# Performance work log

Measured on AMD Instinct MI355X. Metric: run time of the kernel, lower is better.

## Reference

```python
import jax, jax.numpy as jnp
import numpy as np


def setup_inputs() -> dict:
    key = jax.random.key(0)
    ks = jax.random.split(key, 5)
    B, C, H, W = 16, 512, 32, 32
    n_heads, d_k = 4, 128
    return {
        "x": jax.random.normal(ks[0], (B, C, H, W), dtype=jnp.float32),
        "w_proj": jax.random.normal(ks[1], (3 * n_heads * d_k, C), dtype=jnp.float32) * (1.0 / np.sqrt(C)),
        "b_proj": jax.random.normal(ks[2], (3 * n_heads * d_k,), dtype=jnp.float32) * 0.01,
        "w_out": jax.random.normal(ks[3], (C, n_heads * d_k), dtype=jnp.float32) * (1.0 / np.sqrt(n_heads * d_k)),
        "b_out": jax.random.normal(ks[4], (C,), dtype=jnp.float32) * 0.01,
        "n_heads": n_heads,
    }


def reference(x, w_proj, b_proj, w_out, b_out, n_heads):
    B, C, H, W = x.shape
    seq = H * W
    d_k = (w_proj.shape[0] // 3) // n_heads
    scale = d_k ** -0.5

    xs = x.reshape(B, C, seq).transpose(0, 2, 1)          # [B, seq, C]
    qkv = xs @ w_proj.T + b_proj                           # [B, seq, 3*H*d_k]
    qkv = qkv.reshape(B, seq, n_heads, 3 * d_k)
    q, k, v = jnp.split(qkv, 3, axis=-1)                   # each [B, seq, H, d_k]

    attn = jnp.einsum('bihd,bjhd->bijh', q, k) * scale     # [B, seq, seq, H]
    # NOTE: softmax over the QUERY axis (dim=1), faithful to the source quirk.
    attn = jax.nn.softmax(attn, axis=1)

    res = jnp.einsum('bijh,bjhd->bihd', attn, v)           # [B, seq, H, d_k]
    res = res.reshape(B, seq, n_heads * d_k)
    res = res @ w_out.T + b_out + xs                       # residual add
    return res.transpose(0, 2, 1).reshape(B, C, H, W)
```

## Files before the change

### kernel.cpp

```cpp
#include <hip/hip_runtime.h>
#include <hip/hip_bf16.h>
#include <math.h>

#define B_    16
#define CIN   512
#define SEQ   1024
#define NH    4
#define DK    128
#define OUT3  1536
#define SCALE 0.08838834764831845f

typedef __attribute__((ext_vector_type(8))) __bf16 bf16x8;
typedef __attribute__((ext_vector_type(4))) float f32x4;

#define MFMA(a, b, c) __builtin_amdgcn_mfma_f32_16x16x32_bf16((a), (b), (c), 0, 0, 0)

__device__ __forceinline__ ushort f2bf(float f) {
    __hip_bfloat16 h = __float2bfloat16(f);
    return *(ushort*)&h;
}
__device__ __forceinline__ uint pk2(float a, float b) {
    return (uint)f2bf(a) | ((uint)f2bf(b) << 16);
}
__device__ __forceinline__ void g2l16(const ushort* g, ushort* l) {
    __builtin_amdgcn_global_load_lds(
        (const __attribute__((address_space(1))) unsigned int*)g,
        (__attribute__((address_space(3))) unsigned int*)l, 16, 0, 0);
}
__device__ __forceinline__ int xcdswz(int bid, int nwg) {
    return (bid & 7) * (nwg >> 3) + (bid >> 3);
}

__global__ __launch_bounds__(256) void transpose_cast_kernel(
    const float* __restrict__ x, ushort* __restrict__ xt)
{
    __shared__ ushort t[64 * 66];
    const int tid = threadIdx.x;
    const int i0 = blockIdx.x * 64, c0 = blockIdx.y * 64, b = blockIdx.z;

    #pragma unroll
    for (int l = 0; l < 4; ++l) {
        int idx = tid + l * 256;
        int c = idx >> 4, i4 = (idx & 15) << 2;
        float4 v = *(const float4*)&x[((size_t)b * CIN + c0 + c) * SEQ + i0 + i4];
        t[(i4 + 0) * 66 + c] = f2bf(v.x);
        t[(i4 + 1) * 66 + c] = f2bf(v.y);
        t[(i4 + 2) * 66 + c] = f2bf(v.z);
        t[(i4 + 3) * 66 + c] = f2bf(v.w);
    }
    __syncthreads();
    #pragma unroll
    for (int l = 0; l < 4; ++l) {
        int idx = tid + l * 256;
        int i = idx >> 4, c4 = (idx & 15) << 2;
        uint2 p;
        p.x = *(const uint*)&t[i * 66 + c4];
        p.y = *(const uint*)&t[i * 66 + c4 + 2];
        *(uint2*)&xt[((size_t)b * SEQ + i0 + i) * CIN + c0 + c4] = p;
    }
}

__global__ __launch_bounds__(256) void cast_kernel(
    const float* __restrict__ src, ushort* __restrict__ dst, int n4)
{
    int idx = blockIdx.x * 256 + threadIdx.x;
    if (idx < n4) {
        float4 v = *(const float4*)&src[(size_t)idx * 4];
        uint2 p; p.x = pk2(v.x, v.y); p.y = pk2(v.z, v.w);
        *(uint2*)&dst[(size_t)idx * 4] = p;
    }
}

__global__ __launch_bounds__(256) void qkv_kernel(
    const ushort* __restrict__ wbf, const float* __restrict__ bias,
    const ushort* __restrict__ xt,
    ushort* __restrict__ qb, ushort* __restrict__ kb, ushort* __restrict__ vtb)
{
    __shared__ __attribute__((aligned(16))) ushort lds_a[128 * 32];
    __shared__ __attribute__((aligned(16))) ushort lds_b[128 * 32];
    const int tid = threadIdx.x;
    const int lane = tid & 63, wv = tid >> 6;
    const int l15 = lane & 15, l4 = lane >> 4;
    const int wm = wv >> 1, wn = wv & 1;
    const int swz = xcdswz(blockIdx.x, 1536);
    const int o0 = (swz % 12) * 128;
    const int i0 = ((swz / 12) & 7) * 128;
    const int b  = swz / 96;

    f32x4 acc[4][4] = {};
    for (int c0 = 0; c0 < CIN; c0 += 32) {
        __syncthreads();
        #pragma unroll
        for (int l = 0; l < 2; ++l) {
            int chunk = l * 256 + tid;
            int row = chunk >> 2, c = chunk & 3;
            g2l16(&wbf[(size_t)(o0 + row) * CIN + c0 + (c << 3)],
                  &lds_a[(size_t)(l * 256 + wv * 64) * 8]);
        }
        #pragma unroll
        for (int l = 0; l < 2; ++l) {
            int chunk = l * 256 + tid;
            int row = chunk >> 2, c = chunk & 3;
            g2l16(&xt[((size_t)b * SEQ + i0 + row) * CIN + c0 + (c << 3)],
                  &lds_b[(size_t)(l * 256 + wv * 64) * 8]);
        }
        __syncthreads();
        bf16x8 af[4], bfv[4];
        #pragma unroll
        for (int m = 0; m < 4; ++m)
            af[m] = *(const bf16x8*)&lds_a[(wm * 64 + m * 16 + l15) * 32 + (l4 << 3)];
        #pragma unroll
        for (int n = 0; n < 4; ++n)
            bfv[n] = *(const bf16x8*)&lds_b[(wn * 64 + n * 16 + l15) * 32 + (l4 << 3)];
        #pragma unroll
        for (int m = 0; m < 4; ++m)
            #pragma unroll
            for (int n = 0; n < 4; ++n)
                acc[m][n] = MFMA(af[m], bfv[n], acc[m][n]);
    }
    const int h = o0 / 384, which = (o0 % 384) / 128;
    const int bh = b * NH + h;
    #pragma unroll
    for (int m = 0; m < 4; ++m) {
        const int d0 = wm * 64 + m * 16 + (l4 << 2);
        float bia[4];
        #pragma unroll
        for (int r = 0; r < 4; ++r) bia[r] = bias[o0 + d0 + r];
        #pragma unroll
        for (int n = 0; n < 4; ++n) {
            const int i = i0 + wn * 64 + n * 16 + l15;
            float v0 = acc[m][n][0] + bia[0], v1 = acc[m][n][1] + bia[1];
            float v2 = acc[m][n][2] + bia[2], v3 = acc[m][n][3] + bia[3];
            if (which == 2) {
                vtb[((size_t)bh * DK + d0 + 0) * SEQ + i] = f2bf(v0);
                vtb[((size_t)bh * DK + d0 + 1) * SEQ + i] = f2bf(v1);
                vtb[((size_t)bh * DK + d0 + 2) * SEQ + i] = f2bf(v2);
                vtb[((size_t)bh * DK + d0 + 3) * SEQ + i] = f2bf(v3);
            } else {
                ushort* dst = (which == 0) ? qb : kb;
                uint2 p; p.x = pk2(v0, v1); p.y = pk2(v2, v3);
                *(uint2*)&dst[((size_t)bh * SEQ + i) * DK + d0] = p;
            }
        }
    }
}

__global__ __launch_bounds__(256) void stats_kernel(
    const ushort* __restrict__ qb, const ushort* __restrict__ kb,
    float* __restrict__ mstat, float* __restrict__ rstat)
{
    __shared__ __attribute__((aligned(16))) ushort lds_q[64 * 128];
    const int tid = threadIdx.x;
    const int lane = tid & 63, wv = tid >> 6;
    const int l15 = lane & 15, l4 = lane >> 4;
    const int swz = xcdswz(blockIdx.x, 512);
    const int bh = swz >> 3;
    const int j0 = (swz & 7) * 128 + wv * 32;
    const ushort* kbase = kb + (size_t)bh * SEQ * DK;
    const ushort* qbase = qb + (size_t)bh * SEQ * DK;

    bf16x8 kf[2][4];
    #pragma unroll
    for (int m = 0; m < 2; ++m)
        #pragma unroll
        for (int ks = 0; ks < 4; ++ks)
            kf[m][ks] = *(const bf16x8*)&kbase[(size_t)(j0 + m * 16 + l15) * DK
                                               + ks * 32 + (l4 << 3)];
    float mm[2][4], ss[2][4];
    #pragma unroll
    for (int m = 0; m < 2; ++m)
        #pragma unroll
        for (int r = 0; r < 4; ++r) { mm[m][r] = -1e30f; ss[m][r] = 0.0f; }

    for (int it = 0; it < SEQ / 64; ++it) {
        __syncthreads();
        #pragma unroll
        for (int l = 0; l < 4; ++l) {
            int chunk = l * 256 + tid;
            int row = chunk >> 4, c = chunk & 15;
            g2l16(&qbase[(size_t)(it * 64 + row) * DK + ((c ^ (row & 7)) << 3)],
                  &lds_q[(size_t)(l * 256 + wv * 64) * 8]);
        }
        __syncthreads();
        f32x4 sa0[4], sa1[4];
        #pragma unroll
        for (int n = 0; n < 4; ++n) {
            f32x4 a0 = {}, a1 = {};
            #pragma unroll
            for (int ks = 0; ks < 4; ++ks) {
                bf16x8 bq = *(const bf16x8*)&lds_q[(n * 16 + l15) * 128
                                + ((((ks << 2) | l4) ^ (l15 & 7)) << 3)];
                a0 = MFMA(kf[0][ks], bq, a0);
                a1 = MFMA(kf[1][ks], bq, a1);
            }
            sa0[n] = a0; sa1[n] = a1;
        }
        #pragma unroll
        for (int r = 0; r < 4; ++r) {
            {
                float v0 = sa0[0][r] * SCALE, v1 = sa0[1][r] * SCALE;
                float v2 = sa0[2][r] * SCALE, v3 = sa0[3][r] * SCALE;
                float tm = fmaxf(fmaxf(v0, v1), fmaxf(v2, v3));
                float nm = fmaxf(mm[0][r], tm);
                float s4 = __expf(v0 - nm) + __expf(v1 - nm)
                         + __expf(v2 - nm) + __expf(v3 - nm);
                ss[0][r] = ss[0][r] * __expf(mm[0][r] - nm) + s4;
                mm[0][r] = nm;
            }
            {
                float v0 = sa1[0][r] * SCALE, v1 = sa1[1][r] * SCALE;
                float v2 = sa1[2][r] * SCALE, v3 = sa1[3][r] * SCALE;
                float tm = fmaxf(fmaxf(v0, v1), fmaxf(v2, v3));
                float nm = fmaxf(mm[1][r], tm);
                float s4 = __expf(v0 - nm) + __expf(v1 - nm)
                         + __expf(v2 - nm) + __expf(v3 - nm);
                ss[1][r] = ss[1][r] * __expf(mm[1][r] - nm) + s4;
                mm[1][r] = nm;
            }
        }
    }
    #pragma unroll
    for (int m = 0; m < 2; ++m)
        #pragma unroll
        for (int r = 0; r < 4; ++r) {
            float mv = mm[m][r], sv = ss[m][r];
            #pragma unroll
            for (int wmask = 1; wmask < 16; wmask <<= 1) {
                float mo = __shfl_xor(mv, wmask, 64);
                float so = __shfl_xor(sv, wmask, 64);
                float mn = fmaxf(mv, mo);
                sv = sv * __expf(mv - mn) + so * __expf(mo - mn);
                mv = mn;
            }
            if (l15 == 0) {
                int j = j0 + m * 16 + (l4 << 2) + r;
                mstat[(size_t)bh * SEQ + j] = mv;
                rstat[(size_t)bh * SEQ + j] = 1.0f / sv;
            }
        }
}

__global__ __launch_bounds__(256) void attn_kernel(
    const ushort* __restrict__ qb, const ushort* __restrict__ kb,
    const ushort* __restrict__ vtb,
    const float* __restrict__ mstat, const float* __restrict__ rstat,
    ushort* __restrict__ resb)
{
    __shared__ __attribute__((aligned(16))) ushort lds_k[64 * 128];
    __shared__ __attribute__((aligned(16))) ushort lds_vt[128 * 64];
    __shared__ __attribute__((aligned(16))) ushort lds_p[64 * 72];
    const int tid = threadIdx.x;
    const int lane = tid & 63, wv = tid >> 6;
    const int l15 = lane & 15, l4 = lane >> 4;
    const int wj = wv & 1, wi = wv >> 1;
    const int swz = xcdswz(blockIdx.x, 1024);
    const int bh = swz >> 4, b = bh >> 2, h = bh & 3;
    const int i0 = (swz & 15) * 64;
    const ushort* qbase = qb + (size_t)bh * SEQ * DK;
    const ushort* kbase = kb + (size_t)bh * SEQ * DK;
    const ushort* vtbase = vtb + (size_t)bh * DK * SEQ;

    bf16x8 qf[2][4];
    #pragma unroll
    for (int n = 0; n < 2; ++n)
        #pragma unroll
        for (int ks = 0; ks < 4; ++ks)
            qf[n][ks] = *(const bf16x8*)&qbase[(size_t)(i0 + wi * 32 + n * 16 + l15) * DK
                                               + ks * 32 + (l4 << 3)];
    f32x4 oacc[2][4] = {};

    for (int jt = 0; jt < SEQ / 64; ++jt) {
        const int j0 = jt * 64;
        __syncthreads();
        #pragma unroll
        for (int l = 0; l < 4; ++l) {
            int chunk = l * 256 + tid;
            int row = chunk >> 4, c = chunk & 15;
            g2l16(&kbase[(size_t)(j0 + row) * DK + ((c ^ (row & 7)) << 3)],
                  &lds_k[(size_t)(l * 256 + wv * 64) * 8]);
        }
        #pragma unroll
        for (int l = 0; l < 4; ++l) {
            int chunk = l * 256 + tid;
            int row = chunk >> 3, c = chunk & 7;
            g2l16(&vtbase[(size_t)row * SEQ + j0 + ((c ^ (row & 7)) << 3)],
                  &lds_vt[(size_t)(l * 256 + wv * 64) * 8]);
        }
        __syncthreads();
        float mj[2][4], rj[2][4];
        #pragma unroll
        for (int m = 0; m < 2; ++m)
            #pragma unroll
            for (int r = 0; r < 4; ++r) {
                int j = j0 + wj * 32 + m * 16 + (l4 << 2) + r;
                mj[m][r] = mstat[(size_t)bh * SEQ + j];
                rj[m][r] = rstat[(size_t)bh * SEQ + j];
            }
        bf16x8 af[2][4];
        #pragma unroll
        for (int m = 0; m < 2; ++m)
            #pragma unroll
            for (int ks = 0; ks < 4; ++ks)
                af[m][ks] = *(const bf16x8*)&lds_k[(wj * 32 + m * 16 + l15) * 128
                                + ((((ks << 2) | l4) ^ (l15 & 7)) << 3)];
        #pragma unroll
        for (int m = 0; m < 2; ++m)
            #pragma unroll
            for (int n = 0; n < 2; ++n) {
                f32x4 s = {};
                #pragma unroll
                for (int ks = 0; ks < 4; ++ks)
                    s = MFMA(af[m][ks], qf[n][ks], s);
                const int i = wi * 32 + n * 16 + l15;
                float p0 = __expf(s[0] * SCALE - mj[m][0]) * rj[m][0];
                float p1 = __expf(s[1] * SCALE - mj[m][1]) * rj[m][1];
                float p2 = __expf(s[2] * SCALE - mj[m][2]) * rj[m][2];
                float p3 = __expf(s[3] * SCALE - mj[m][3]) * rj[m][3];
                uint2 pp; pp.x = pk2(p0, p1); pp.y = pk2(p2, p3);
                *(uint2*)&lds_p[i * 72 + wj * 32 + m * 16 + (l4 << 2)] = pp;
            }
        __syncthreads();
        #pragma unroll
        for (int ks = 0; ks < 2; ++ks) {
            bf16x8 va0 = *(const bf16x8*)&lds_vt[(wv * 32 + l15) * 64
                            + ((((ks << 2) | l4) ^ (l15 & 7)) << 3)];
            bf16x8 va1 = *(const bf16x8*)&lds_vt[(wv * 32 + 16 + l15) * 64
                            + ((((ks << 2) | l4) ^ (l15 & 7)) << 3)];
            #pragma unroll
            for (int n = 0; n < 4; ++n) {
                bf16x8 pb = *(const bf16x8*)&lds_p[(n * 16 + l15) * 72
                                + ks * 32 + (l4 << 3)];
                oacc[0][n] = MFMA(va0, pb, oacc[0][n]);
                oacc[1][n] = MFMA(va1, pb, oacc[1][n]);
            }
        }
    }
    #pragma unroll
    for (int m = 0; m < 2; ++m)
        #pragma unroll
        for (int n = 0; n < 4; ++n) {
            const int i = i0 + n * 16 + l15;
            const int d = wv * 32 + m * 16 + (l4 << 2);
            uint2 p;
            p.x = pk2(oacc[m][n][0], oacc[m][n][1]);
            p.y = pk2(oacc[m][n][2], oacc[m][n][3]);
            *(uint2*)&resb[((size_t)b * SEQ + i) * (NH * DK) + h * DK + d] = p;
        }
}

__global__ __launch_bounds__(256) void outproj_kernel(
    const ushort* __restrict__ resb, const ushort* __restrict__ woutbf,
    const float* __restrict__ bout, const float* __restrict__ x,
    float* __restrict__ out)
{
    __shared__ __attribute__((aligned(16))) ushort lds_a[128 * 32];
    __shared__ __attribute__((aligned(16))) ushort lds_b[128 * 32];
    const int tid = threadIdx.x;
    const int lane = tid & 63, wv = tid >> 6;
    const int l15 = lane & 15, l4 = lane >> 4;
    const int wm = wv >> 1, wn = wv & 1;
    const int swz = xcdswz(blockIdx.x, 512);
    const int i0 = (swz & 7) * 128;
    const int c0 = ((swz >> 3) & 3) * 128;
    const int b  = swz >> 5;

    f32x4 acc[4][4] = {};
    for (int k0 = 0; k0 < NH * DK; k0 += 32) {
        __syncthreads();
        #pragma unroll
        for (int l = 0; l < 2; ++l) {
            int chunk = l * 256 + tid;
            int row = chunk >> 2, c = chunk & 3;
            g2l16(&woutbf[(size_t)(c0 + row) * (NH * DK) + k0 + (c << 3)],
                  &lds_a[(size_t)(l * 256 + wv * 64) * 8]);
        }
        #pragma unroll
        for (int l = 0; l < 2; ++l) {
            int chunk = l * 256 + tid;
            int row = chunk >> 2, c = chunk & 3;
            g2l16(&resb[((size_t)b * SEQ + i0 + row) * (NH * DK) + k0 + (c << 3)],
                  &lds_b[(size_t)(l * 256 + wv * 64) * 8]);
        }
        __syncthreads();
        bf16x8 af[4], bfv[4];
        #pragma unroll
        for (int m = 0; m < 4; ++m)
            af[m] = *(const bf16x8*)&lds_a[(wm * 64 + m * 16 + l15) * 32 + (l4 << 3)];
        #pragma unroll
        for (int n = 0; n < 4; ++n)
            bfv[n] = *(const bf16x8*)&lds_b[(wn * 64 + n * 16 + l15) * 32 + (l4 << 3)];
        #pragma unroll
        for (int m = 0; m < 4; ++m)
            #pragma unroll
            for (int n = 0; n < 4; ++n)
                acc[m][n] = MFMA(af[m], bfv[n], acc[m][n]);
    }
    #pragma unroll
    for (int m = 0; m < 4; ++m) {
        const int cb = c0 + wm * 64 + m * 16 + (l4 << 2);
        float bia[4];
        #pragma unroll
        for (int r = 0; r < 4; ++r) bia[r] = bout[cb + r];
        #pragma unroll
        for (int n = 0; n < 4; ++n) {
            const int i = i0 + wn * 64 + n * 16 + l15;
            #pragma unroll
            for (int r = 0; r < 4; ++r) {
                size_t off = ((size_t)b * CIN + cb + r) * SEQ + i;
                out[off] = acc[m][n][r] + bia[r] + x[off];
            }
        }
    }
}

extern "C" void kernel_launch(void* const* d_in, const int* in_sizes, int n_in,
                              void* d_out, int out_size, void* d_ws, size_t ws_size,
                              hipStream_t stream) {
    const float* x      = (const float*)d_in[0];
    const float* w_proj = (const float*)d_in[1];
    const float* b_proj = (const float*)d_in[2];
    const float* w_out  = (const float*)d_in[3];
    const float* b_out  = (const float*)d_in[4];

    const size_t xtE = (size_t)B_ * SEQ * CIN;
    const size_t qkE = (size_t)B_ * NH * SEQ * DK;
    ushort* xt    = (ushort*)d_ws;
    ushort* qb    = xt + xtE;
    ushort* kb    = qb + qkE;
    ushort* vtb   = kb + qkE;
    float*  mstat = (float*)(vtb + qkE);
    float*  rstat = mstat + (size_t)B_ * NH * SEQ;
    ushort* resb  = (ushort*)(rstat + (size_t)B_ * NH * SEQ);
    ushort* wobf  = resb + (size_t)B_ * SEQ * (NH * DK);
    ushort* wpbf  = resb;
    float*  out   = (float*)d_out;

    transpose_cast_kernel<<<dim3(SEQ / 64, CIN / 64, B_), 256, 0, stream>>>(x, xt);
    cast_kernel<<<dim3(768), 256, 0, stream>>>(w_proj, wpbf, 196608);
    cast_kernel<<<dim3(256), 256, 0, stream>>>(w_out, wobf, 65536);
    qkv_kernel<<<dim3(1536), 256, 0, stream>>>(wpbf, b_proj, xt, qb, kb, vtb);
    stats_kernel<<<dim3(512), 256, 0, stream>>>(qb, kb, mstat, rstat);
    attn_kernel<<<dim3(1024), 256, 0, stream>>>(qb, kb, vtb, mstat, rstat, resb);
    outproj_kernel<<<dim3(512), 256, 0, stream>>>(resb, wobf, b_out, x, out);
}
```

Before: 259.7 us.

## Double-buffer LDS staging in GEMM and stats kernels, fold softmax stats into logsumexp

The QKV and output projection GEMMs and the stats kernel now double-buffer their LDS tiles, issuing the next tile's global-to-LDS copy before computing on the current one, which removes one barrier per iteration. The attention kernel splits K and V staging so the next K tile loads during the PV MFMA phase, and it wraps the MFMA sections in s_setprio hints. The per-column max and reciprocal sum are merged into one logsumexp value, which removes a load and a multiply per element. The extra LDS buffers double shared memory use in the GEMMs and may lower occupancy.

Result: faster. 250.2 us (-3.7%).

```diff
diff --git a/kernel.cpp b/kernel.cpp
--- a/kernel.cpp
+++ b/kernel.cpp
@@ -76,8 +76,10 @@
     const ushort* __restrict__ xt,
     ushort* __restrict__ qb, ushort* __restrict__ kb, ushort* __restrict__ vtb)
 {
-    __shared__ __attribute__((aligned(16))) ushort lds_a[128 * 32];
-    __shared__ __attribute__((aligned(16))) ushort lds_b[128 * 32];
+    __shared__ __attribute__((aligned(16))) ushort lds_a0[128 * 32];
+    __shared__ __attribute__((aligned(16))) ushort lds_a1[128 * 32];
+    __shared__ __attribute__((aligned(16))) ushort lds_b0[128 * 32];
+    __shared__ __attribute__((aligned(16))) ushort lds_b1[128 * 32];
     const int tid = threadIdx.x;
     const int lane = tid & 63, wv = tid >> 6;
     const int l15 = lane & 15, l4 = lane >> 4;
@@ -87,36 +89,45 @@
     const int i0 = ((swz / 12) & 7) * 128;
     const int b  = swz / 96;
 
-    f32x4 acc[4][4] = {};
-    for (int c0 = 0; c0 < CIN; c0 += 32) {
-        __syncthreads();
+    auto stage = [&](int c0, ushort* la, ushort* lb) {
         #pragma unroll
         for (int l = 0; l < 2; ++l) {
             int chunk = l * 256 + tid;
             int row = chunk >> 2, c = chunk & 3;
             g2l16(&wbf[(size_t)(o0 + row) * CIN + c0 + (c << 3)],
-                  &lds_a[(size_t)(l * 256 + wv * 64) * 8]);
+                  &la[(size_t)(l * 256 + wv * 64) * 8]);
         }
         #pragma unroll
         for (int l = 0; l < 2; ++l) {
             int chunk = l * 256 + tid;
             int row = chunk >> 2, c = chunk & 3;
             g2l16(&xt[((size_t)b * SEQ + i0 + row) * CIN + c0 + (c << 3)],
-                  &lds_b[(size_t)(l * 256 + wv * 64) * 8]);
-        }
-        __syncthreads();
+                  &lb[(size_t)(l * 256 + wv * 64) * 8]);
+        }
+    };
+
+    f32x4 acc[4][4] = {};
+    stage(0, lds_a0, lds_b0);
+    __syncthreads();
+    for (int it = 0; it < CIN / 32; ++it) {
+        const ushort* la = (it & 1) ? lds_a1 : lds_a0;
+        const ushort* lb = (it & 1) ? lds_b1 : lds_b0;
+        if (it + 1 < CIN / 32)
+            stage((it + 1) * 32, (it & 1) ? lds_a0 : lds_a1,
+                                 (it & 1) ? lds_b0 : lds_b1);
         bf16x8 af[4], bfv[4];
         #pragma unroll
         for (int m = 0; m < 4; ++m)
-            af[m] = *(const bf16x8*)&lds_a[(wm * 64 + m * 16 + l15) * 32 + (l4 << 3)];
+            af[m] = *(const bf16x8*)&la[(wm * 64 + m * 16 + l15) * 32 + (l4 << 3)];
         #pragma unroll
         for (int n = 0; n < 4; ++n)
-            bfv[n] = *(const bf16x8*)&lds_b[(wn * 64 + n * 16 + l15) * 32 + (l4 << 3)];
+            bfv[n] = *(const bf16x8*)&lb[(wn * 64 + n * 16 + l15) * 32 + (l4 << 3)];
         #pragma unroll
         for (int m = 0; m < 4; ++m)
             #pragma unroll
             for (int n = 0; n < 4; ++n)
                 acc[m][n] = MFMA(af[m], bfv[n], acc[m][n]);
+        __syncthreads();
     }
     const int h = o0 / 384, which = (o0 % 384) / 128;
     const int bh = b * NH + h;
@@ -147,9 +158,10 @@
 
 __global__ __launch_bounds__(256) void stats_kernel(
     const ushort* __restrict__ qb, const ushort* __restrict__ kb,
-    float* __restrict__ mstat, float* __restrict__ rstat)
-{
-    __shared__ __attribute__((aligned(16))) ushort lds_q[64 * 128];
+    float* __restrict__ cstat)
+{
+    __shared__ __attribute__((aligned(16))) ushort lds_q0[64 * 128];
+    __shared__ __attribute__((aligned(16))) ushort lds_q1[64 * 128];
     const int tid = threadIdx.x;
     const int lane = tid & 63, wv = tid >> 6;
     const int l15 = lane & 15, l4 = lane >> 4;
@@ -159,6 +171,16 @@
     const ushort* kbase = kb + (size_t)bh * SEQ * DK;
     const ushort* qbase = qb + (size_t)bh * SEQ * DK;
 
+    auto stageQ = [&](int it, ushort* dst) {
+        #pragma unroll
+        for (int l = 0; l < 4; ++l) {
+            int chunk = l * 256 + tid;
+            int row = chunk >> 4, c = chunk & 15;
+            g2l16(&qbase[(size_t)(it * 64 + row) * DK + ((c ^ (row & 7)) << 3)],
+                  &dst[(size_t)(l * 256 + wv * 64) * 8]);
+        }
+    };
+
     bf16x8 kf[2][4];
     #pragma unroll
     for (int m = 0; m < 2; ++m)
@@ -172,29 +194,27 @@
         #pragma unroll
         for (int r = 0; r < 4; ++r) { mm[m][r] = -1e30f; ss[m][r] = 0.0f; }
 
+    stageQ(0, lds_q0);
+    __syncthreads();
     for (int it = 0; it < SEQ / 64; ++it) {
-        __syncthreads();
-        #pragma unroll
-        for (int l = 0; l < 4; ++l) {
-            int chunk = l * 256 + tid;
-            int row = chunk >> 4, c = chunk & 15;
-            g2l16(&qbase[(size_t)(it * 64 + row) * DK + ((c ^ (row & 7)) << 3)],
-                  &lds_q[(size_t)(l * 256 + wv * 64) * 8]);
-        }
-        __syncthreads();
+        const ushort* lq = (it & 1) ? lds_q1 : lds_q0;
+        if (it + 1 < SEQ / 64)
+            stageQ(it + 1, (it & 1) ? lds_q0 : lds_q1);
         f32x4 sa0[4], sa1[4];
+        __builtin_amdgcn_s_setprio(1);
         #pragma unroll
         for (int n = 0; n < 4; ++n) {
             f32x4 a0 = {}, a1 = {};
             #pragma unroll
             for (int ks = 0; ks < 4; ++ks) {
-                bf16x8 bq = *(const bf16x8*)&lds_q[(n * 16 + l15) * 128
+                bf16x8 bq = *(const bf16x8*)&lq[(n * 16 + l15) * 128
                                 + ((((ks << 2) | l4) ^ (l15 & 7)) << 3)];
                 a0 = MFMA(kf[0][ks], bq, a0);
                 a1 = MFMA(kf[1][ks], bq, a1);
             }
             sa0[n] = a0; sa1[n] = a1;
         }
+        __builtin_amdgcn_s_setprio(0);
         #pragma unroll
         for (int r = 0; r < 4; ++r) {
             {
@@ -218,6 +238,7 @@
                 mm[1][r] = nm;
             }
         }
+        __syncthreads();
     }
     #pragma unroll
     for (int m = 0; m < 2; ++m)
@@ -234,16 +255,14 @@
             }
             if (l15 == 0) {
                 int j = j0 + m * 16 + (l4 << 2) + r;
-                mstat[(size_t)bh * SEQ + j] = mv;
-                rstat[(size_t)bh * SEQ + j] = 1.0f / sv;
+                cstat[(size_t)bh * SEQ + j] = mv + __logf(sv);
             }
         }
 }
 
 __global__ __launch_bounds__(256) void attn_kernel(
     const ushort* __restrict__ qb, const ushort* __restrict__ kb,
-    const ushort* __restrict__ vtb,
-    const float* __restrict__ mstat, const float* __restrict__ rstat,
+    const ushort* __restrict__ vtb, const float* __restrict__ cstat,
     ushort* __restrict__ resb)
 {
     __shared__ __attribute__((aligned(16))) ushort lds_k[64 * 128];
@@ -259,6 +278,26 @@
     const ushort* qbase = qb + (size_t)bh * SEQ * DK;
     const ushort* kbase = kb + (size_t)bh * SEQ * DK;
     const ushort* vtbase = vtb + (size_t)bh * DK * SEQ;
+    const float* cbase = cstat + (size_t)bh * SEQ;
+
+    auto stageK = [&](int j0t) {
+        #pragma unroll
+        for (int l = 0; l < 4; ++l) {
+            int chunk = l * 256 + tid;
+            int row = chunk >> 4, c = chunk & 15;
+            g2l16(&kbase[(size_t)(j0t + row) * DK + ((c ^ (row & 7)) << 3)],
+                  &lds_k[(size_t)(l * 256 + wv * 64) * 8]);
+        }
+    };
+    auto stageVt = [&](int j0t) {
+        #pragma unroll
+        for (int l = 0; l < 4; ++l) {
+            int chunk = l * 256 + tid;
+            int row = chunk >> 3, c = chunk & 7;
+            g2l16(&vtbase[(size_t)row * SEQ + j0t + ((c ^ (row & 7)) << 3)],
+                  &lds_vt[(size_t)(l * 256 + wv * 64) * 8]);
+        }
+    };
 
     bf16x8 qf[2][4];
     #pragma unroll
@@ -269,33 +308,15 @@
                                                + ks * 32 + (l4 << 3)];
     f32x4 oacc[2][4] = {};
 
+    stageK(0);
+    __syncthreads();
     for (int jt = 0; jt < SEQ / 64; ++jt) {
         const int j0 = jt * 64;
-        __syncthreads();
-        #pragma unroll
-        for (int l = 0; l < 4; ++l) {
-            int chunk = l * 256 + tid;
-            int row = chunk >> 4, c = chunk & 15;
-            g2l16(&kbase[(size_t)(j0 + row) * DK + ((c ^ (row & 7)) << 3)],
-                  &lds_k[(size_t)(l * 256 + wv * 64) * 8]);
-        }
-        #pragma unroll
-        for (int l = 0; l < 4; ++l) {
-            int chunk = l * 256 + tid;
-            int row = chunk >> 3, c = chunk & 7;
-            g2l16(&vtbase[(size_t)row * SEQ + j0 + ((c ^ (row & 7)) << 3)],
-                  &lds_vt[(size_t)(l * 256 + wv * 64) * 8]);
-        }
-        __syncthreads();
-        float mj[2][4], rj[2][4];
-        #pragma unroll
-        for (int m = 0; m < 2; ++m)
-            #pragma unroll
-            for (int r = 0; r < 4; ++r) {
-                int j = j0 + wj * 32 + m * 16 + (l4 << 2) + r;
-                mj[m][r] = mstat[(size_t)bh * SEQ + j];
-                rj[m][r] = rstat[(size_t)bh * SEQ + j];
-            }
+        stageVt(j0);
+        float4 cs0 = *(const float4*)&cbase[j0 + wj * 32 + (l4 << 2)];
+        float4 cs1 = *(const float4*)&cbase[j0 + wj * 32 + 16 + (l4 << 2)];
+        float cj[2][4] = {{cs0.x, cs0.y, cs0.z, cs0.w},
+                          {cs1.x, cs1.y, cs1.z, cs1.w}};
         bf16x8 af[2][4];
         #pragma unroll
         for (int m = 0; m < 2; ++m)
@@ -303,6 +324,7 @@
             for (int ks = 0; ks < 4; ++ks)
                 af[m][ks] = *(const bf16x8*)&lds_k[(wj * 32 + m * 16 + l15) * 128
                                 + ((((ks << 2) | l4) ^ (l15 & 7)) << 3)];
+        __builtin_amdgcn_s_setprio(1);
         #pragma unroll
         for (int m = 0; m < 2; ++m)
             #pragma unroll
@@ -312,14 +334,17 @@
                 for (int ks = 0; ks < 4; ++ks)
                     s = MFMA(af[m][ks], qf[n][ks], s);
                 const int i = wi * 32 + n * 16 + l15;
-                float p0 = __expf(s[0] * SCALE - mj[m][0]) * rj[m][0];
-                float p1 = __expf(s[1] * SCALE - mj[m][1]) * rj[m][1];
-                float p2 = __expf(s[2] * SCALE - mj[m][2]) * rj[m][2];
-                float p3 = __expf(s[3] * SCALE - mj[m][3]) * rj[m][3];
+                float p0 = __expf(s[0] * SCALE - cj[m][0]);
+                float p1 = __expf(s[1] * SCALE - cj[m][1]);
+                float p2 = __expf(s[2] * SCALE - cj[m][2]);
+                float p3 = __expf(s[3] * SCALE - cj[m][3]);
                 uint2 pp; pp.x = pk2(p0, p1); pp.y = pk2(p2, p3);
                 *(uint2*)&lds_p[i * 72 + wj * 32 + m * 16 + (l4 << 2)] = pp;
             }
+        __builtin_amdgcn_s_setprio(0);
         __syncthreads();
+        if (jt + 1 < SEQ / 64) stageK(j0 + 64);
+        __builtin_amdgcn_s_setprio(1);
         #pragma unroll
         for (int ks = 0; ks < 2; ++ks) {
             bf16x8 va0 = *(const bf16x8*)&lds_vt[(wv * 32 + l15) * 64
@@ -334,6 +359,8 @@
                 oacc[1][n] = MFMA(va1, pb, oacc[1][n]);
             }
         }
+        __builtin_amdgcn_s_setprio(0);
+        __syncthreads();
     }
     #pragma unroll
     for (int m = 0; m < 2; ++m)
@@ -353,8 +380,10 @@
     const float* __restrict__ bout, const float* __restrict__ x,
     float* __restrict__ out)
 {
-    __shared__ __attribute__((aligned(16))) ushort lds_a[128 * 32];
-    __shared__ __attribute__((aligned(16))) ushort lds_b[128 * 32];
+    __shared__ __attribute__((aligned(16))) ushort lds_a0[128 * 32];
+    __shared__ __attribute__((aligned(16))) ushort lds_a1[128 * 32];
+    __shared__ __attribute__((aligned(16))) ushort lds_b0[128 * 32];
+    __shared__ __attribute__((aligned(16))) ushort lds_b1[128 * 32];
     const int tid = threadIdx.x;
     const int lane = tid & 63, wv = tid >> 6;
     const int l15 = lane & 15, l4 = lane >> 4;
@@ -364,36 +393,45 @@
     const int c0 = ((swz >> 3) & 3) * 128;
     const int b  = swz >> 5;
 
-    f32x4 acc[4][4] = {};
-    for (int k0 = 0; k0 < NH * DK; k0 += 32) {
-        __syncthreads();
+    auto stage = [&](int k0, ushort* la, ushort* lb) {
         #pragma unroll
         for (int l = 0; l < 2; ++l) {
             int chunk = l * 256 + tid;
             int row = chunk >> 2, c = chunk & 3;
             g2l16(&woutbf[(size_t)(c0 + row) * (NH * DK) + k0 + (c << 3)],
-                  &lds_a[(size_t)(l * 256 + wv * 64) * 8]);
+                  &la[(size_t)(l * 256 + wv * 64) * 8]);
         }
         #pragma unroll
         for (int l = 0; l < 2; ++l) {
             int chunk = l * 256 + tid;
             int row = chunk >> 2, c = chunk & 3;
             g2l16(&resb[((size_t)b * SEQ + i0 + row) * (NH * DK) + k0 + (c << 3)],
-                  &lds_b[(size_t)(l * 256 + wv * 64) * 8]);
-        }
-        __syncthreads();
+                  &lb[(size_t)(l * 256 + wv * 64) * 8]);
+        }
+    };
+
+    f32x4 acc[4][4] = {};
+    stage(0, lds_a0, lds_b0);
+    __syncthreads();
+    for (int it = 0; it < (NH * DK) / 32; ++it) {
+        const ushort* la = (it & 1) ? lds_a1 : lds_a0;
+        const ushort* lb = (it & 1) ? lds_b1 : lds_b0;
+        if (it + 1 < (NH * DK) / 32)
+            stage((it + 1) * 32, (it & 1) ? lds_a0 : lds_a1,
+                                 (it & 1) ? lds_b0 : lds_b1);
         bf16x8 af[4], bfv[4];
         #pragma unroll
         for (int m = 0; m < 4; ++m)
-            af[m] = *(const bf16x8*)&lds_a[(wm * 64 + m * 16 + l15) * 32 + (l4 << 3)];
+            af[m] = *(const bf16x8*)&la[(wm * 64 + m * 16 + l15) * 32 + (l4 << 3)];
         #pragma unroll
         for (int n = 0; n < 4; ++n)
-            bfv[n] = *(const bf16x8*)&lds_b[(wn * 64 + n * 16 + l15) * 32 + (l4 << 3)];
+            bfv[n] = *(const bf16x8*)&lb[(wn * 64 + n * 16 + l15) * 32 + (l4 << 3)];
         #pragma unroll
         for (int m = 0; m < 4; ++m)
             #pragma unroll
             for (int n = 0; n < 4; ++n)
                 acc[m][n] = MFMA(af[m], bfv[n], acc[m][n]);
+        __syncthreads();
     }
     #pragma unroll
     for (int m = 0; m < 4; ++m) {
@@ -428,9 +466,8 @@
     ushort* qb    = xt + xtE;
     ushort* kb    = qb + qkE;
     ushort* vtb   = kb + qkE;
-    float*  mstat = (float*)(vtb + qkE);
-    float*  rstat = mstat + (size_t)B_ * NH * SEQ;
-    ushort* resb  = (ushort*)(rstat + (size_t)B_ * NH * SEQ);
+    float*  cstat = (float*)(vtb + qkE);
+    ushort* resb  = (ushort*)(cstat + 2 * (size_t)B_ * NH * SEQ);
     ushort* wobf  = resb + (size_t)B_ * SEQ * (NH * DK);
     ushort* wpbf  = resb;
     float*  out   = (float*)d_out;
@@ -439,7 +476,7 @@
     cast_kernel<<<dim3(768), 256, 0, stream>>>(w_proj, wpbf, 196608);
     cast_kernel<<<dim3(256), 256, 0, stream>>>(w_out, wobf, 65536);
     qkv_kernel<<<dim3(1536), 256, 0, stream>>>(wpbf, b_proj, xt, qb, kb, vtb);
-    stats_kernel<<<dim3(512), 256, 0, stream>>>(qb, kb, mstat, rstat);
-    attn_kernel<<<dim3(1024), 256, 0, stream>>>(qb, kb, vtb, mstat, rstat, resb);
+    stats_kernel<<<dim3(512), 256, 0, stream>>>(qb, kb, cstat);
+    attn_kernel<<<dim3(1024), 256, 0, stream>>>(qb, kb, vtb, cstat, resb);
     outproj_kernel<<<dim3(512), 256, 0, stream>>>(resb, wobf, b_out, x, out);
 }
```
